# Performance work log

Hardware: AMD Instinct MI355X
Metric: run time of the kernel (lower is better)

The kernel has to match this reference:

```python
import math
import jax, jax.numpy as jnp
import numpy as np

C = 64
GRID = 2

def _conv1x1(x, W, b):
    # 1x1 conv == channel-mixing matmul: [B,C,H,W] x [O,C] -> [B,O,H,W]
    return jnp.einsum('bchw,oc->bohw', x, W) + b[None, :, None, None]

def setup_inputs() -> dict:
    key = jax.random.key(0)
    ks = jax.random.split(key, 11)
    s = 1.0 / math.sqrt(C)
    def w(k):
        return jax.random.normal(k, (C, C), dtype=jnp.float32) * s
    def bias(k):
        return jax.random.normal(k, (C,), dtype=jnp.float32) * 0.02
    return {
        'x': jax.random.normal(ks[0], (2, C, 128, 128), dtype=jnp.float32),
        'Wq': w(ks[1]), 'bq': bias(ks[2]),
        'Wk': w(ks[3]), 'bk': bias(ks[4]),
        'Wa': w(ks[5]), 'ba': bias(ks[6]),
        'Wb': w(ks[7]), 'bb': bias(ks[8]),
        'Wo': w(ks[9]), 'bo': bias(ks[10]),
    }

def reference(x, Wq, bq, Wk, bk, Wa, ba, Wb, bb, Wo, bo):
    B, c, H, W = x.shape
    g = GRID
    rh, rw = H // g, W // g  # H,W chosen divisible by grid -> no reflect pad
    N = rh * rw
    R = g * g

    q = _conv1x1(x, Wq, bq)
    k = _conv1x1(x, Wk, bk)
    a = _conv1x1(x, Wa, ba)
    bt = _conv1x1(x, Wb, bb)

    def regionize(t):
        # [B,C,H,W] -> [B, R, C, N] with N = rh*rw row-major per region
        return t.reshape(B, c, g, rh, g, rw).transpose(0, 2, 4, 1, 3, 5).reshape(B, R, c, N)

    qr, kr, ar, br = regionize(q), regionize(k), regionize(a), regionize(bt)

    # attn[b,r,n,m] = softmax_m( q^T k / sqrt(C) )
    attn = jax.nn.softmax(jnp.einsum('brcn,brcm->brnm', qr, kr) / math.sqrt(c), axis=-1)

    # out_r = alpha @ attn + beta @ attn^T
    out = (jnp.einsum('brcj,brjm->brcm', ar, attn)
           + jnp.einsum('brcj,brmj->brcm', br, attn))

    # [B,R,C,N] -> [B,C,H,W]
    out = out.reshape(B, g, g, c, rh, rw).transpose(0, 3, 1, 4, 2, 5).reshape(B, c, H, W)
    return _conv1x1(out, Wo, bo)
```

## Files before the change

kernel.cpp:

```cpp
#include <hip/hip_runtime.h>


typedef __attribute__((ext_vector_type(8)))  short bf16x8;
typedef __attribute__((ext_vector_type(16))) float f32x16;

#define MFMA32(a, b, c) __builtin_amdgcn_mfma_f32_32x32x16_bf16(a, b, c, 0, 0, 0)

constexpr int REG_ELEMS = 4096 * 64;
constexpr size_t QP_OFF  = 0;
constexpr size_t KP_OFF  = 4u  << 20;
constexpr size_t ATL_OFF = 8u  << 20;
constexpr size_t BTL_OFF = 12u << 20;
constexpr size_t OUTP_OFF= 16u << 20;
constexpr size_t LNV_OFF = 20u << 20;

constexpr float QSCALE = 0.18033688011112042f;

__device__ __forceinline__ short f2bf(float f) {
    union { float f; unsigned u; } v; v.f = f;
    unsigned r = v.u + 0x7fffu + ((v.u >> 16) & 1u);
    return (short)(r >> 16);
}
__device__ __forceinline__ float bf2f(short s) {
    union { unsigned u; float f; } v; v.u = ((unsigned)(unsigned short)s) << 16;
    return v.f;
}
__device__ __forceinline__ unsigned fbits(float f) {
    union { float f; unsigned u; } v; v.f = f; return v.u;
}
__device__ __forceinline__ unsigned pack_trunc(float e0, float e1) {
    return __builtin_amdgcn_perm(fbits(e1), fbits(e0), 0x07060302u);
}
__device__ __forceinline__ f32x16 zero16() {
    f32x16 z;
    #pragma unroll
    for (int i = 0; i < 16; ++i) z[i] = 0.f;
    return z;
}
__device__ __forceinline__ float fexp2(float x) {
#if __has_builtin(__builtin_amdgcn_exp2f)
    return __builtin_amdgcn_exp2f(x);
#else
    return exp2f(x);
#endif
}
__device__ __forceinline__ void permswap32(unsigned& a, unsigned& b, bool hi) {
#if __has_builtin(__builtin_amdgcn_permlane32_swap)
    auto r = __builtin_amdgcn_permlane32_swap(a, b, false, false);
    a = r[0]; b = r[1];
#elif __has_builtin(__builtin_amdgcn_permlane32_swap_b32)
    auto r = __builtin_amdgcn_permlane32_swap_b32(a, b, false, false);
    a = r[0]; b = r[1];
#else
    unsigned ax = (unsigned)__shfl_xor((int)a, 32);
    unsigned bx = (unsigned)__shfl_xor((int)b, 32);
    unsigned na = hi ? bx : a;
    unsigned nb = hi ? b  : ax;
    a = na; b = nb;
#endif
}

typedef __attribute__((address_space(1))) const unsigned char as1_t;
typedef __attribute__((address_space(3))) unsigned char as3_t;
__device__ __forceinline__ void stage16(const void* g, void* l) {
    __builtin_amdgcn_global_load_lds((as1_t*)g, (as3_t*)l, 16, 0, 0);
}

__global__ __launch_bounds__(256) void k_conv_in(
    const float* __restrict__ x,
    const float* __restrict__ Wq, const float* __restrict__ bq,
    const float* __restrict__ Wk, const float* __restrict__ bk,
    const float* __restrict__ Wa, const float* __restrict__ ba,
    const float* __restrict__ Wb, const float* __restrict__ bb,
    char* __restrict__ ws)
{
    const int tid  = threadIdx.x;
    const int blk  = blockIdx.x;
    const int wseg = blk & 1;
    const int h    = (blk >> 1) & 127;
    const int b    = blk >> 8;
    const int br   = b * 4 + (h >> 6) * 2 + wseg;
    const int n0   = (h & 63) * 64;

    __shared__ float xs[64][68];
    __shared__ short trans[2][64][72];

    const float* xp = x + ((size_t)b * 64 * 16384) + (size_t)h * 128 + wseg * 64;
    #pragma unroll
    for (int r = 0; r < 4; ++r) {
        int idx = r * 256 + tid;
        int c   = idx >> 4;
        int w4  = (idx & 15) << 2;
        *(float4*)&xs[c][w4] = *(const float4*)(xp + (size_t)c * 16384 + w4);
    }
    __syncthreads();

    const int lane = tid & 63;
    const int wid  = tid >> 6;
    const int col  = lane & 31;
    const int l5   = lane >> 5;
    const int pH   = wid & 1;
    const int oH   = wid >> 1;
    const int px   = pH * 32 + col;
    const int oc   = oH * 32 + col;

    bf16x8 xhi[4], xlo[4];
    #pragma unroll
    for (int s = 0; s < 4; ++s) {
        union { bf16x8 v; short sh[8]; } uh, ul;
        #pragma unroll
        for (int e = 0; e < 8; ++e) {
            float xv = xs[s * 16 + l5 * 8 + e][px];
            short hh = f2bf(xv);
            uh.sh[e] = hh;
            ul.sh[e] = f2bf(xv - bf2f(hh));
        }
        xhi[s] = uh.v; xlo[s] = ul.v;
    }

    #pragma unroll
    for (int mat = 0; mat < 4; ++mat) {
        const float* Wsel = (mat == 0) ? Wq : (mat == 1) ? Wk : (mat == 2) ? Wa : Wb;
        const float* bsel = (mat == 0) ? bq : (mat == 1) ? bk : (mat == 2) ? ba : bb;

        bf16x8 whi[4], wlo[4];
        const float* wrow = Wsel + (size_t)oc * 64;
        #pragma unroll
        for (int s = 0; s < 4; ++s) {
            float4 f0 = *(const float4*)(wrow + s * 16 + l5 * 8);
            float4 f1 = *(const float4*)(wrow + s * 16 + l5 * 8 + 4);
            float wf[8] = { f0.x, f0.y, f0.z, f0.w, f1.x, f1.y, f1.z, f1.w };
            union { bf16x8 v; short sh[8]; } uh, ul;
            #pragma unroll
            for (int e = 0; e < 8; ++e) {
                short hh = f2bf(wf[e]);
                uh.sh[e] = hh;
                ul.sh[e] = f2bf(wf[e] - bf2f(hh));
            }
            whi[s] = uh.v; wlo[s] = ul.v;
        }

        f32x16 d = zero16();
        #pragma unroll
        for (int s = 0; s < 4; ++s) {
            d = MFMA32(xhi[s], whi[s], d);
            d = MFMA32(xhi[s], wlo[s], d);
            d = MFMA32(xlo[s], whi[s], d);
        }

        const float bias = bsel[oc];
        if (mat < 2) {
            const float sc = (mat == 0) ? QSCALE : 1.0f;
            #pragma unroll
            for (int r = 0; r < 16; ++r) {
                int pxl = pH * 32 + (r & 3) + 8 * (r >> 2) + 4 * l5;
                trans[mat][pxl][oc] = f2bf((d[r] + bias) * sc);
            }
        } else {
            short* base = (short*)(ws + (mat == 2 ? ATL_OFF : BTL_OFF))
                          + (size_t)br * REG_ELEMS;
            const int sw   = (oc >> 1) & 3;
            const int tile = (n0 >> 5) + pH;
            #pragma unroll
            for (int q = 0; q < 4; ++q) {
                short tmp4[4];
                #pragma unroll
                for (int rr = 0; rr < 4; ++rr) tmp4[rr] = f2bf(d[4 * q + rr] + bias);
                int segp = q ^ sw;
                short* p = base + (size_t)tile * 2048 + oc * 32 + segp * 8 + 4 * l5;
                *(uint2*)p = *(uint2*)tmp4;
            }
        }
    }
    __syncthreads();

    #pragma unroll
    for (int rep = 0; rep < 4; ++rep) {
        int idx  = rep * 256 + tid;
        int mat2 = idx >> 9;
        int row  = (idx >> 3) & 63;
        int seg  = idx & 7;
        short* dst = (short*)(ws + (mat2 ? KP_OFF : QP_OFF))
                     + (size_t)br * REG_ELEMS + (size_t)(n0 + row) * 64
                     + (seg ^ (row & 7)) * 8;
        *(uint4*)dst = *(uint4*)&trans[mat2][row][seg * 8];
    }
}

__global__ __launch_bounds__(256, 2) void k_stats(char* __restrict__ ws)
{
    const int tid  = threadIdx.x;
    const int br   = blockIdx.x & 7;
    const int nt   = blockIdx.x >> 3;
    const int lane = tid & 63;
    const int w    = tid >> 6;
    const int wn   = w & 1;
    const int wi   = w >> 1;
    const int col  = lane & 31;
    const int l5   = lane >> 5;

    const short* Qb  = (const short*)(ws + QP_OFF) + (size_t)br * REG_ELEMS;
    const char*  Kbb = ws + KP_OFF + (size_t)br * REG_ELEMS * 2;

    __shared__ __align__(16) char smem[17408];

    const int nrow = nt * 64 + wn * 32 + col;
    bf16x8 afr[4];
    #pragma unroll
    for (int s = 0; s < 4; ++s)
        afr[s] = *(const bf16x8*)(Qb + (size_t)nrow * 64 + (((2*s+l5) ^ (col & 7)) * 8));

    float sm[16];
    #pragma unroll
    for (int r = 0; r < 16; ++r) sm[r] = 0.f;

    {
        const char* g = Kbb + (size_t)w * 2048 + lane * 16;
        char* l = smem + w * 2048;
        stage16(g, l); stage16(g + 1024, l + 1024);
    }

    #pragma unroll 2
    for (int slab = 0; slab < 64; ++slab) {
        __syncthreads();
        if (slab + 1 < 64) {
            const char* g = Kbb + (size_t)(slab + 1) * 8192 + w * 2048 + lane * 16;
            char* l = smem + ((slab + 1) & 1) * 8192 + w * 2048;
            stage16(g, l); stage16(g + 1024, l + 1024);
        }
        const short* Ks = (const short*)(smem + (slab & 1) * 8192);
        f32x16 d = zero16();
        #pragma unroll
        for (int s = 0; s < 4; ++s) {
            bf16x8 bf = *(const bf16x8*)(Ks + (wi * 32 + col) * 64
                                         + ((2*s+l5) ^ (col & 7)) * 8);
            d = MFMA32(afr[s], bf, d);
        }
        #pragma unroll
        for (int r = 0; r < 16; ++r) sm[r] += fexp2(d[r]);
    }

    #pragma unroll
    for (int off = 1; off < 32; off <<= 1)
        #pragma unroll
        for (int r = 0; r < 16; ++r) sm[r] += __shfl_xor(sm[r], off);

    __syncthreads();
    float* Lred = (float*)(smem + 16384);
    float* Larr = (float*)(smem + 16896);
    if (col == 0) {
        #pragma unroll
        for (int r = 0; r < 16; ++r)
            Lred[w * 32 + ((r & 3) + 8 * (r >> 2) + 4 * l5)] = sm[r];
    }
    __syncthreads();
    if (tid < 64) {
        int wn2 = tid >> 5, nl = tid & 31;
        float L = Lred[wn2 * 32 + nl] + Lred[(wn2 + 2) * 32 + nl];
        float li = 1.0f / L;
        Larr[tid] = li;
        ((float*)(ws + LNV_OFF))[(size_t)br * 4096 + nt * 64 + tid] = li;
    }
    __syncthreads();

    short* Ab = (short*)(ws + ATL_OFF) + (size_t)br * REG_ELEMS + (size_t)nt * 4096;
    #pragma unroll
    for (int rep = 0; rep < 2; ++rep) {
        int id = rep * 256 + tid;
        int t = id >> 8, c = (id >> 2) & 63, s = id & 3;
        int sg = s ^ ((c >> 1) & 3);
        int jl = t * 32 + sg * 8;
        short* p = Ab + (size_t)t * 2048 + c * 32 + s * 8;
        uint4 v = *(uint4*)p;
        short* sp = (short*)&v;
        short o[8];
        #pragma unroll
        for (int e = 0; e < 8; ++e) o[e] = f2bf(bf2f(sp[e]) * Larr[jl + e]);
        *(uint4*)p = *(uint4*)o;
    }
}

__global__ __launch_bounds__(256, 2) void k_attn(char* __restrict__ ws)
{
    const int tid  = threadIdx.x;
    const int br   = blockIdx.x & 7;
    const int mt   = blockIdx.x >> 3;
    const int lane = tid & 63;
    const int w    = tid >> 6;
    const int wm   = w & 1;
    const int wj   = w >> 1;
    const int col  = lane & 31;
    const int l5   = lane >> 5;
    const bool hi  = (l5 != 0);

    const char* Qbb = ws + QP_OFF  + (size_t)br * REG_ELEMS * 2;
    const char* Kbb = ws + KP_OFF  + (size_t)br * REG_ELEMS * 2;
    const char* Abb = ws + ATL_OFF + (size_t)br * REG_ELEMS * 2;
    const char* Bbb = ws + BTL_OFF + (size_t)br * REG_ELEMS * 2;
    const float* Lnv = (const float*)(ws + LNV_OFF) + (size_t)br * 4096;
    short* OutPb    = (short*)(ws + OUTP_OFF) + (size_t)br * REG_ELEMS;

    __shared__ __align__(16) char smem[32768];

    const int mrow = mt * 64 + wm * 32 + col;
    const short* msrc = (const short*)(wj == 0 ? Kbb : Qbb) + (size_t)mrow * 64;
    bf16x8 mf[4];
    #pragma unroll
    for (int s = 0; s < 4; ++s)
        mf[s] = *(const bf16x8*)(msrc + ((2*s+l5) ^ (col & 7)) * 8);

    f32x16 accL = zero16(), accH = zero16();

    const char* gsb = (w == 0) ? Qbb : (w == 1) ? Kbb : (w == 2) ? Abb : Bbb;

    {
        const char* g = gsb + lane * 16;
        char* l = smem + w * 4096 + lane * 16;
        #pragma unroll
        for (int i = 0; i < 4; ++i) stage16(g + i * 1024, l + i * 1024);
    }

    #pragma unroll 2
    for (int slab = 0; slab < 128; ++slab) {
        __syncthreads();
        if (slab + 1 < 128) {
            const char* g = gsb + (size_t)(slab + 1) * 4096 + lane * 16;
            char* l = smem + ((slab + 1) & 1) * 16384 + w * 4096 + lane * 16;
            #pragma unroll
            for (int i = 0; i < 4; ++i) stage16(g + i * 1024, l + i * 1024);
        }
        const char* sb = smem + (slab & 1) * 16384;
        const short* js = (const short*)(sb + (wj == 0 ? 0 : 4096));
        const short* ts = (const short*)(sb + (wj == 0 ? 8192 : 12288));

        f32x16 d = zero16();
        #pragma unroll
        for (int s = 0; s < 4; ++s) {
            bf16x8 a = *(const bf16x8*)(js + col * 64 + ((2*s+l5) ^ (col & 7)) * 8);
            d = MFMA32(a, mf[s], d);
        }

        unsigned Wp[8];
        #pragma unroll
        for (int q = 0; q < 4; ++q) {
            Wp[2*q]   = pack_trunc(fexp2(d[4*q]),   fexp2(d[4*q+1]));
            Wp[2*q+1] = pack_trunc(fexp2(d[4*q+2]), fexp2(d[4*q+3]));
        }

        #pragma unroll
        for (int k16 = 0; k16 < 2; ++k16) {
            unsigned u0 = Wp[4*k16+0], u1 = Wp[4*k16+1];
            unsigned u2 = Wp[4*k16+2], u3 = Wp[4*k16+3];
            permswap32(u0, u2, hi);
            permswap32(u1, u3, hi);
            union { uint4 u; bf16x8 v; } fr;
            fr.u.x = u0; fr.u.y = u1; fr.u.z = u2; fr.u.w = u3;

            const int swz = ((2*k16 + l5) ^ ((col >> 1) & 3)) * 8;
            bf16x8 bL = *(const bf16x8*)(ts + col * 32 + swz);
            bf16x8 bH = *(const bf16x8*)(ts + (col + 32) * 32 + swz);
            accL = MFMA32(fr.v, bL, accL);
            accH = MFMA32(fr.v, bH, accH);
        }
    }

    __syncthreads();
    float* red = (float*)smem;
    if (wj == 0) {
        #pragma unroll
        for (int r = 0; r < 16; ++r) {
            int ml = wm * 32 + (r & 3) + 8 * (r >> 2) + 4 * l5;
            red[ml * 68 + col]      = accL[r];
            red[ml * 68 + 32 + col] = accH[r];
        }
    }
    __syncthreads();
    if (wj == 1) {
        #pragma unroll
        for (int r = 0; r < 16; ++r) {
            int ml = wm * 32 + (r & 3) + 8 * (r >> 2) + 4 * l5;
            float li = Lnv[mt * 64 + ml];
            red[ml * 68 + col]      += li * accL[r];
            red[ml * 68 + 32 + col] += li * accH[r];
        }
    }
    __syncthreads();
    {
        const int m  = tid >> 2;
        const int c0 = (tid & 3) * 16;
        const float* rp = red + m * 68 + c0;
        uint4 p0, p1;
        p0.x = pack_trunc(rp[0],  rp[1]);  p0.y = pack_trunc(rp[2],  rp[3]);
        p0.z = pack_trunc(rp[4],  rp[5]);  p0.w = pack_trunc(rp[6],  rp[7]);
        p1.x = pack_trunc(rp[8],  rp[9]);  p1.y = pack_trunc(rp[10], rp[11]);
        p1.z = pack_trunc(rp[12], rp[13]); p1.w = pack_trunc(rp[14], rp[15]);
        short* orow = OutPb + (size_t)(mt * 64 + m) * 64 + c0;
        *(uint4*)orow       = p0;
        *(uint4*)(orow + 8) = p1;
    }
}

__global__ __launch_bounds__(64) void k_conv_out(
    const char* __restrict__ ws,
    const float* __restrict__ Wo, const float* __restrict__ bo,
    float* __restrict__ out)
{
    const int lane = threadIdx.x;
    const int br   = blockIdx.x & 7;
    const int nt   = blockIdx.x >> 3;
    const int col  = lane & 31;
    const int l5   = lane >> 5;

    const short* OutPb = (const short*)(ws + OUTP_OFF) + (size_t)br * REG_ELEMS;

    bf16x8 afr[4];
    const short* arow = OutPb + (size_t)(nt * 32 + col) * 64 + l5 * 8;
    #pragma unroll
    for (int s = 0; s < 4; ++s) afr[s] = *(const bf16x8*)(arow + s * 16);

    bf16x8 bw[2][4];
    #pragma unroll
    for (int oh = 0; oh < 2; ++oh) {
        const float* wrow = Wo + (size_t)(oh * 32 + col) * 64 + l5 * 8;
        #pragma unroll
        for (int s = 0; s < 4; ++s) {
            float4 f0 = *(const float4*)(wrow + s * 16);
            float4 f1 = *(const float4*)(wrow + s * 16 + 4);
            union { bf16x8 v; short sh[8]; } u;
            u.sh[0] = f2bf(f0.x); u.sh[1] = f2bf(f0.y);
            u.sh[2] = f2bf(f0.z); u.sh[3] = f2bf(f0.w);
            u.sh[4] = f2bf(f1.x); u.sh[5] = f2bf(f1.y);
            u.sh[6] = f2bf(f1.z); u.sh[7] = f2bf(f1.w);
            bw[oh][s] = u.v;
        }
    }

    f32x16 d0 = zero16(), d1 = zero16();
    #pragma unroll
    for (int s = 0; s < 4; ++s) {
        d0 = MFMA32(afr[s], bw[0][s], d0);
        d1 = MFMA32(afr[s], bw[1][s], d1);
    }

    const int b  = br >> 2;
    const int gi = (br >> 1) & 1;
    const int gj = br & 1;

    #pragma unroll
    for (int oh = 0; oh < 2; ++oh) {
        const int oc = oh * 32 + col;
        const float bias = bo[oc];
        const f32x16& d = oh ? d1 : d0;
        #pragma unroll
        for (int q = 0; q < 4; ++q) {
            int nloc = 8 * q + 4 * l5;
            int nreg = nt * 32 + nloc;
            int wp   = nreg & 63;
            int ip   = nreg >> 6;
            float4 v = make_float4(d[4*q+0] + bias, d[4*q+1] + bias,
                                   d[4*q+2] + bias, d[4*q+3] + bias);
            float* op = out + ((size_t)(b * 64 + oc)) * 16384
                        + (size_t)(gi * 64 + ip) * 128 + gj * 64 + wp;
            *(float4*)op = v;
        }
    }
}

extern "C" void kernel_launch(void* const* d_in, const int* in_sizes, int n_in,
                              void* d_out, int out_size, void* d_ws, size_t ws_size,
                              hipStream_t stream)
{
    const float* x  = (const float*)d_in[0];
    const float* Wq = (const float*)d_in[1];
    const float* bq = (const float*)d_in[2];
    const float* Wk = (const float*)d_in[3];
    const float* bk = (const float*)d_in[4];
    const float* Wa = (const float*)d_in[5];
    const float* ba = (const float*)d_in[6];
    const float* Wb = (const float*)d_in[7];
    const float* bb = (const float*)d_in[8];
    const float* Wo = (const float*)d_in[9];
    const float* bo = (const float*)d_in[10];
    char* ws   = (char*)d_ws;
    float* out = (float*)d_out;

    hipLaunchKernelGGL(k_conv_in,  dim3(512),  dim3(256), 0, stream,
                       x, Wq, bq, Wk, bk, Wa, ba, Wb, bb, ws);
    hipLaunchKernelGGL(k_stats,    dim3(512),  dim3(256), 0, stream, ws);
    hipLaunchKernelGGL(k_attn,     dim3(512),  dim3(256), 0, stream, ws);
    hipLaunchKernelGGL(k_conv_out, dim3(1024), dim3(64),  0, stream,
                       ws, Wo, bo, out);
}
```

Before: 206.1 us.

## Split key dimension across two blocks in stats and attention kernels

Doubles the grid of k_stats and k_attn by splitting the 4096-long key/j range into two halves. Partial softmax denominators are written separately and merged by a new small k_stats2 kernel. The in-place rescaling of the alpha tile by 1/L is dropped; that normalization is instead applied inside k_attn to the exp weights on the alpha path. Two partial attention outputs are summed in k_conv_out via extra MFMAs. This raises occupancy on a 256-CU device (512 blocks was only 2 per CU), at the cost of an extra launch, double output buffers and per-slab Lnv loads.

```diff
diff --git a/kernel.cpp b/kernel.cpp
--- a/kernel.cpp
+++ b/kernel.cpp
@@ -7,12 +7,14 @@
 #define MFMA32(a, b, c) __builtin_amdgcn_mfma_f32_32x32x16_bf16(a, b, c, 0, 0, 0)
 
 constexpr int REG_ELEMS = 4096 * 64;
-constexpr size_t QP_OFF  = 0;
-constexpr size_t KP_OFF  = 4u  << 20;
-constexpr size_t ATL_OFF = 8u  << 20;
-constexpr size_t BTL_OFF = 12u << 20;
-constexpr size_t OUTP_OFF= 16u << 20;
-constexpr size_t LNV_OFF = 20u << 20;
+constexpr size_t QP_OFF    = 0;
+constexpr size_t KP_OFF    = 4u  << 20;
+constexpr size_t ATL_OFF   = 8u  << 20;
+constexpr size_t BTL_OFF   = 12u << 20;
+constexpr size_t OUTP0_OFF = 16u << 20;
+constexpr size_t OUTP1_OFF = 20u << 20;
+constexpr size_t LNV_OFF   = 24u << 20;
+constexpr size_t LPART_OFF = (24u << 20) + (128u << 10);
 
 constexpr float QSCALE = 0.18033688011112042f;
 
@@ -191,7 +193,8 @@
 {
     const int tid  = threadIdx.x;
     const int br   = blockIdx.x & 7;
-    const int nt   = blockIdx.x >> 3;
+    const int nt   = (blockIdx.x >> 3) & 63;
+    const int ms   = blockIdx.x >> 9;
     const int lane = tid & 63;
     const int w    = tid >> 6;
     const int wn   = w & 1;
@@ -200,9 +203,10 @@
     const int l5   = lane >> 5;
 
     const short* Qb  = (const short*)(ws + QP_OFF) + (size_t)br * REG_ELEMS;
-    const char*  Kbb = ws + KP_OFF + (size_t)br * REG_ELEMS * 2;
-
-    __shared__ __align__(16) char smem[17408];
+    const char*  Kbb = ws + KP_OFF + (size_t)br * REG_ELEMS * 2
+                       + (size_t)ms * 262144;
+
+    __shared__ __align__(16) char smem[16896];
 
     const int nrow = nt * 64 + wn * 32 + col;
     bf16x8 afr[4];
@@ -221,9 +225,9 @@
     }
 
     #pragma unroll 2
-    for (int slab = 0; slab < 64; ++slab) {
+    for (int slab = 0; slab < 32; ++slab) {
         __syncthreads();
-        if (slab + 1 < 64) {
+        if (slab + 1 < 32) {
             const char* g = Kbb + (size_t)(slab + 1) * 8192 + w * 2048 + lane * 16;
             char* l = smem + ((slab + 1) & 1) * 8192 + w * 2048;
             stage16(g, l); stage16(g + 1024, l + 1024);
@@ -247,7 +251,6 @@
 
     __syncthreads();
     float* Lred = (float*)(smem + 16384);
-    float* Larr = (float*)(smem + 16896);
     if (col == 0) {
         #pragma unroll
         for (int r = 0; r < 16; ++r)
@@ -257,34 +260,24 @@
     if (tid < 64) {
         int wn2 = tid >> 5, nl = tid & 31;
         float L = Lred[wn2 * 32 + nl] + Lred[(wn2 + 2) * 32 + nl];
-        float li = 1.0f / L;
-        Larr[tid] = li;
-        ((float*)(ws + LNV_OFF))[(size_t)br * 4096 + nt * 64 + tid] = li;
-    }
-    __syncthreads();
-
-    short* Ab = (short*)(ws + ATL_OFF) + (size_t)br * REG_ELEMS + (size_t)nt * 4096;
-    #pragma unroll
-    for (int rep = 0; rep < 2; ++rep) {
-        int id = rep * 256 + tid;
-        int t = id >> 8, c = (id >> 2) & 63, s = id & 3;
-        int sg = s ^ ((c >> 1) & 3);
-        int jl = t * 32 + sg * 8;
-        short* p = Ab + (size_t)t * 2048 + c * 32 + s * 8;
-        uint4 v = *(uint4*)p;
-        short* sp = (short*)&v;
-        short o[8];
-        #pragma unroll
-        for (int e = 0; e < 8; ++e) o[e] = f2bf(bf2f(sp[e]) * Larr[jl + e]);
-        *(uint4*)p = *(uint4*)o;
-    }
+        ((float*)(ws + LPART_OFF))[(size_t)ms * 32768 + (size_t)br * 4096
+                                   + nt * 64 + tid] = L;
+    }
+}
+
+__global__ __launch_bounds__(256) void k_stats2(char* __restrict__ ws)
+{
+    const int i = blockIdx.x * 256 + threadIdx.x;
+    const float* Lp = (const float*)(ws + LPART_OFF);
+    ((float*)(ws + LNV_OFF))[i] = 1.0f / (Lp[i] + Lp[32768 + i]);
 }
 
 __global__ __launch_bounds__(256, 2) void k_attn(char* __restrict__ ws)
 {
     const int tid  = threadIdx.x;
     const int br   = blockIdx.x & 7;
-    const int mt   = blockIdx.x >> 3;
+    const int mt   = (blockIdx.x >> 3) & 63;
+    const int js   = blockIdx.x >> 9;
     const int lane = tid & 63;
     const int w    = tid >> 6;
     const int wm   = w & 1;
@@ -298,7 +291,7 @@
     const char* Abb = ws + ATL_OFF + (size_t)br * REG_ELEMS * 2;
     const char* Bbb = ws + BTL_OFF + (size_t)br * REG_ELEMS * 2;
     const float* Lnv = (const float*)(ws + LNV_OFF) + (size_t)br * 4096;
-    short* OutPb    = (short*)(ws + OUTP_OFF) + (size_t)br * REG_ELEMS;
+    short* OutPb = (short*)(ws + (js ? OUTP1_OFF : OUTP0_OFF)) + (size_t)br * REG_ELEMS;
 
     __shared__ __align__(16) char smem[32768];
 
@@ -311,7 +304,8 @@
 
     f32x16 accL = zero16(), accH = zero16();
 
-    const char* gsb = (w == 0) ? Qbb : (w == 1) ? Kbb : (w == 2) ? Abb : Bbb;
+    const char* gsb = ((w == 0) ? Qbb : (w == 1) ? Kbb : (w == 2) ? Abb : Bbb)
+                      + (size_t)js * 262144;
 
     {
         const char* g = gsb + lane * 16;
@@ -321,30 +315,40 @@
     }
 
     #pragma unroll 2
-    for (int slab = 0; slab < 128; ++slab) {
+    for (int slab = 0; slab < 64; ++slab) {
         __syncthreads();
-        if (slab + 1 < 128) {
+        if (slab + 1 < 64) {
             const char* g = gsb + (size_t)(slab + 1) * 4096 + lane * 16;
             char* l = smem + ((slab + 1) & 1) * 16384 + w * 4096 + lane * 16;
             #pragma unroll
             for (int i = 0; i < 4; ++i) stage16(g + i * 1024, l + i * 1024);
         }
         const char* sb = smem + (slab & 1) * 16384;
-        const short* js = (const short*)(sb + (wj == 0 ? 0 : 4096));
-        const short* ts = (const short*)(sb + (wj == 0 ? 8192 : 12288));
+        const short* js_ = (const short*)(sb + (wj == 0 ? 0 : 4096));
+        const short* ts  = (const short*)(sb + (wj == 0 ? 8192 : 12288));
 
         f32x16 d = zero16();
         #pragma unroll
         for (int s = 0; s < 4; ++s) {
-            bf16x8 a = *(const bf16x8*)(js + col * 64 + ((2*s+l5) ^ (col & 7)) * 8);
+            bf16x8 a = *(const bf16x8*)(js_ + col * 64 + ((2*s+l5) ^ (col & 7)) * 8);
             d = MFMA32(a, mf[s], d);
         }
 
         unsigned Wp[8];
-        #pragma unroll
-        for (int q = 0; q < 4; ++q) {
-            Wp[2*q]   = pack_trunc(fexp2(d[4*q]),   fexp2(d[4*q+1]));
-            Wp[2*q+1] = pack_trunc(fexp2(d[4*q+2]), fexp2(d[4*q+3]));
+        if (wj == 0) {
+            const int jbase = (js * 64 + slab) * 32;
+            #pragma unroll
+            for (int q = 0; q < 4; ++q) {
+                float4 Lq = *(const float4*)(Lnv + jbase + 8 * q + 4 * l5);
+                Wp[2*q]   = pack_trunc(fexp2(d[4*q])   * Lq.x, fexp2(d[4*q+1]) * Lq.y);
+                Wp[2*q+1] = pack_trunc(fexp2(d[4*q+2]) * Lq.z, fexp2(d[4*q+3]) * Lq.w);
+            }
+        } else {
+            #pragma unroll
+            for (int q = 0; q < 4; ++q) {
+                Wp[2*q]   = pack_trunc(fexp2(d[4*q]),   fexp2(d[4*q+1]));
+                Wp[2*q+1] = pack_trunc(fexp2(d[4*q+2]), fexp2(d[4*q+3]));
+            }
         }
 
         #pragma unroll
@@ -411,12 +415,16 @@
     const int col  = lane & 31;
     const int l5   = lane >> 5;
 
-    const short* OutPb = (const short*)(ws + OUTP_OFF) + (size_t)br * REG_ELEMS;
-
-    bf16x8 afr[4];
-    const short* arow = OutPb + (size_t)(nt * 32 + col) * 64 + l5 * 8;
-    #pragma unroll
-    for (int s = 0; s < 4; ++s) afr[s] = *(const bf16x8*)(arow + s * 16);
+    const short* O0 = (const short*)(ws + OUTP0_OFF) + (size_t)br * REG_ELEMS;
+    const short* O1 = (const short*)(ws + OUTP1_OFF) + (size_t)br * REG_ELEMS;
+
+    bf16x8 af0[4], af1[4];
+    const size_t aoff = (size_t)(nt * 32 + col) * 64 + l5 * 8;
+    #pragma unroll
+    for (int s = 0; s < 4; ++s) {
+        af0[s] = *(const bf16x8*)(O0 + aoff + s * 16);
+        af1[s] = *(const bf16x8*)(O1 + aoff + s * 16);
+    }
 
     bf16x8 bw[2][4];
     #pragma unroll
@@ -438,8 +446,10 @@
     f32x16 d0 = zero16(), d1 = zero16();
     #pragma unroll
     for (int s = 0; s < 4; ++s) {
-        d0 = MFMA32(afr[s], bw[0][s], d0);
-        d1 = MFMA32(afr[s], bw[1][s], d1);
+        d0 = MFMA32(af0[s], bw[0][s], d0);
+        d0 = MFMA32(af1[s], bw[0][s], d0);
+        d1 = MFMA32(af0[s], bw[1][s], d1);
+        d1 = MFMA32(af1[s], bw[1][s], d1);
     }
 
     const int b  = br >> 2;
@@ -486,8 +496,9 @@
 
     hipLaunchKernelGGL(k_conv_in,  dim3(512),  dim3(256), 0, stream,
                        x, Wq, bq, Wk, bk, Wa, ba, Wb, bb, ws);
-    hipLaunchKernelGGL(k_stats,    dim3(512),  dim3(256), 0, stream, ws);
-    hipLaunchKernelGGL(k_attn,     dim3(512),  dim3(256), 0, stream, ws);
+    hipLaunchKernelGGL(k_stats,    dim3(1024), dim3(256), 0, stream, ws);
+    hipLaunchKernelGGL(k_stats2,   dim3(128),  dim3(256), 0, stream, ws);
+    hipLaunchKernelGGL(k_attn,     dim3(1024), dim3(256), 0, stream, ws);
     hipLaunchKernelGGL(k_conv_out, dim3(1024), dim3(64),  0, stream,
                        ws, Wo, bo, out);
 }
```

Measured after the change: 212.0 us. 2.8% more time.

## Fold inverse-sum scaling of alpha into attn kernel; pack conv_out into 256-thread blocks

Applied to the files above, without the earlier changes.

The k_stats kernel no longer rescales the alpha tile in global memory by 1/L. Only the inverse row sums are stored, and k_attn multiplies the exp weights by them for the wj==0 warps (alpha path) before packing to bf16. This removes a read-modify-write pass over the alpha buffer and an extra barrier, at the cost of extra global loads and multiplies inside the attention loop. Separately, k_conv_out now packs four 64-thread tiles into each 256-thread block to cut the block count.

```diff
diff --git a/kernel.cpp b/kernel.cpp
--- a/kernel.cpp
+++ b/kernel.cpp
@@ -202,7 +202,7 @@
     const short* Qb  = (const short*)(ws + QP_OFF) + (size_t)br * REG_ELEMS;
     const char*  Kbb = ws + KP_OFF + (size_t)br * REG_ELEMS * 2;
 
-    __shared__ __align__(16) char smem[17408];
+    __shared__ __align__(16) char smem[16896];
 
     const int nrow = nt * 64 + wn * 32 + col;
     bf16x8 afr[4];
@@ -247,7 +247,6 @@
 
     __syncthreads();
     float* Lred = (float*)(smem + 16384);
-    float* Larr = (float*)(smem + 16896);
     if (col == 0) {
         #pragma unroll
         for (int r = 0; r < 16; ++r)
@@ -257,26 +256,7 @@
     if (tid < 64) {
         int wn2 = tid >> 5, nl = tid & 31;
         float L = Lred[wn2 * 32 + nl] + Lred[(wn2 + 2) * 32 + nl];
-        float li = 1.0f / L;
-        Larr[tid] = li;
-        ((float*)(ws + LNV_OFF))[(size_t)br * 4096 + nt * 64 + tid] = li;
-    }
-    __syncthreads();
-
-    short* Ab = (short*)(ws + ATL_OFF) + (size_t)br * REG_ELEMS + (size_t)nt * 4096;
-    #pragma unroll
-    for (int rep = 0; rep < 2; ++rep) {
-        int id = rep * 256 + tid;
-        int t = id >> 8, c = (id >> 2) & 63, s = id & 3;
-        int sg = s ^ ((c >> 1) & 3);
-        int jl = t * 32 + sg * 8;
-        short* p = Ab + (size_t)t * 2048 + c * 32 + s * 8;
-        uint4 v = *(uint4*)p;
-        short* sp = (short*)&v;
-        short o[8];
-        #pragma unroll
-        for (int e = 0; e < 8; ++e) o[e] = f2bf(bf2f(sp[e]) * Larr[jl + e]);
-        *(uint4*)p = *(uint4*)o;
+        ((float*)(ws + LNV_OFF))[(size_t)br * 4096 + nt * 64 + tid] = 1.0f / L;
     }
 }
 
@@ -341,10 +321,20 @@
         }
 
         unsigned Wp[8];
-        #pragma unroll
-        for (int q = 0; q < 4; ++q) {
-            Wp[2*q]   = pack_trunc(fexp2(d[4*q]),   fexp2(d[4*q+1]));
-            Wp[2*q+1] = pack_trunc(fexp2(d[4*q+2]), fexp2(d[4*q+3]));
+        if (wj == 0) {
+            const int jbase = slab * 32;
+            #pragma unroll
+            for (int q = 0; q < 4; ++q) {
+                float4 Lq = *(const float4*)(Lnv + jbase + 8 * q + 4 * l5);
+                Wp[2*q]   = pack_trunc(fexp2(d[4*q])   * Lq.x, fexp2(d[4*q+1]) * Lq.y);
+                Wp[2*q+1] = pack_trunc(fexp2(d[4*q+2]) * Lq.z, fexp2(d[4*q+3]) * Lq.w);
+            }
+        } else {
+            #pragma unroll
+            for (int q = 0; q < 4; ++q) {
+                Wp[2*q]   = pack_trunc(fexp2(d[4*q]),   fexp2(d[4*q+1]));
+                Wp[2*q+1] = pack_trunc(fexp2(d[4*q+2]), fexp2(d[4*q+3]));
+            }
         }
 
         #pragma unroll
@@ -400,14 +390,17 @@
     }
 }
 
-__global__ __launch_bounds__(64) void k_conv_out(
+__global__ __launch_bounds__(256) void k_conv_out(
     const char* __restrict__ ws,
     const float* __restrict__ Wo, const float* __restrict__ bo,
     float* __restrict__ out)
 {
-    const int lane = threadIdx.x;
-    const int br   = blockIdx.x & 7;
-    const int nt   = blockIdx.x >> 3;
+    const int tid  = threadIdx.x;
+    const int lane = tid & 63;
+    const int sub  = tid >> 6;
+    const int blk  = blockIdx.x;
+    const int br   = blk & 7;
+    const int nt   = (blk >> 3) * 4 + sub;
     const int col  = lane & 31;
     const int l5   = lane >> 5;
 
@@ -484,10 +477,10 @@
     char* ws   = (char*)d_ws;
     float* out = (float*)d_out;
 
-    hipLaunchKernelGGL(k_conv_in,  dim3(512),  dim3(256), 0, stream,
+    hipLaunchKernelGGL(k_conv_in,  dim3(512), dim3(256), 0, stream,
                        x, Wq, bq, Wk, bk, Wa, ba, Wb, bb, ws);
-    hipLaunchKernelGGL(k_stats,    dim3(512),  dim3(256), 0, stream, ws);
-    hipLaunchKernelGGL(k_attn,     dim3(512),  dim3(256), 0, stream, ws);
-    hipLaunchKernelGGL(k_conv_out, dim3(1024), dim3(64),  0, stream,
+    hipLaunchKernelGGL(k_stats,    dim3(512), dim3(256), 0, stream, ws);
+    hipLaunchKernelGGL(k_attn,     dim3(512), dim3(256), 0, stream, ws);
+    hipLaunchKernelGGL(k_conv_out, dim3(256), dim3(256), 0, stream,
                        ws, Wo, bo, out);
 }
```

Measured after the change: 238.0 us. 15.5% more time.

## Split attention reduction over j into two halves, combine partials in output conv

Applied to the files above, without the earlier changes.

The attention kernel's 128-slab reduction is split into two halves across twice as many blocks, each writing partial outputs to separate workspace buffers. The output conv kernel now loads both partials and accumulates them via extra MFMAs, and is relaunched with 256-thread blocks covering four tiles each. This raises parallelism from 512 to 1024 attention blocks to better fill the GPU, at the cost of extra partial-output traffic and bf16 rounding of each partial before summation.

```diff
diff --git a/kernel.cpp b/kernel.cpp
--- a/kernel.cpp
+++ b/kernel.cpp
@@ -7,12 +7,13 @@
 #define MFMA32(a, b, c) __builtin_amdgcn_mfma_f32_32x32x16_bf16(a, b, c, 0, 0, 0)
 
 constexpr int REG_ELEMS = 4096 * 64;
-constexpr size_t QP_OFF  = 0;
-constexpr size_t KP_OFF  = 4u  << 20;
-constexpr size_t ATL_OFF = 8u  << 20;
-constexpr size_t BTL_OFF = 12u << 20;
-constexpr size_t OUTP_OFF= 16u << 20;
-constexpr size_t LNV_OFF = 20u << 20;
+constexpr size_t QP_OFF    = 0;
+constexpr size_t KP_OFF    = 4u  << 20;
+constexpr size_t ATL_OFF   = 8u  << 20;
+constexpr size_t BTL_OFF   = 12u << 20;
+constexpr size_t OUTP0_OFF = 16u << 20;
+constexpr size_t OUTP1_OFF = 20u << 20;
+constexpr size_t LNV_OFF   = 24u << 20;
 
 constexpr float QSCALE = 0.18033688011112042f;
 
@@ -284,7 +285,8 @@
 {
     const int tid  = threadIdx.x;
     const int br   = blockIdx.x & 7;
-    const int mt   = blockIdx.x >> 3;
+    const int mt   = (blockIdx.x >> 3) & 63;
+    const int js   = blockIdx.x >> 9;
     const int lane = tid & 63;
     const int w    = tid >> 6;
     const int wm   = w & 1;
@@ -298,7 +300,7 @@
     const char* Abb = ws + ATL_OFF + (size_t)br * REG_ELEMS * 2;
     const char* Bbb = ws + BTL_OFF + (size_t)br * REG_ELEMS * 2;
     const float* Lnv = (const float*)(ws + LNV_OFF) + (size_t)br * 4096;
-    short* OutPb    = (short*)(ws + OUTP_OFF) + (size_t)br * REG_ELEMS;
+    short* OutPb = (short*)(ws + (js ? OUTP1_OFF : OUTP0_OFF)) + (size_t)br * REG_ELEMS;
 
     __shared__ __align__(16) char smem[32768];
 
@@ -311,7 +313,8 @@
 
     f32x16 accL = zero16(), accH = zero16();
 
-    const char* gsb = (w == 0) ? Qbb : (w == 1) ? Kbb : (w == 2) ? Abb : Bbb;
+    const char* gsb = ((w == 0) ? Qbb : (w == 1) ? Kbb : (w == 2) ? Abb : Bbb)
+                      + (size_t)js * 262144;
 
     {
         const char* g = gsb + lane * 16;
@@ -321,22 +324,22 @@
     }
 
     #pragma unroll 2
-    for (int slab = 0; slab < 128; ++slab) {
+    for (int slab = 0; slab < 64; ++slab) {
         __syncthreads();
-        if (slab + 1 < 128) {
+        if (slab + 1 < 64) {
             const char* g = gsb + (size_t)(slab + 1) * 4096 + lane * 16;
             char* l = smem + ((slab + 1) & 1) * 16384 + w * 4096 + lane * 16;
             #pragma unroll
             for (int i = 0; i < 4; ++i) stage16(g + i * 1024, l + i * 1024);
         }
         const char* sb = smem + (slab & 1) * 16384;
-        const short* js = (const short*)(sb + (wj == 0 ? 0 : 4096));
+        const short* jr = (const short*)(sb + (wj == 0 ? 0 : 4096));
         const short* ts = (const short*)(sb + (wj == 0 ? 8192 : 12288));
 
         f32x16 d = zero16();
         #pragma unroll
         for (int s = 0; s < 4; ++s) {
-            bf16x8 a = *(const bf16x8*)(js + col * 64 + ((2*s+l5) ^ (col & 7)) * 8);
+            bf16x8 a = *(const bf16x8*)(jr + col * 64 + ((2*s+l5) ^ (col & 7)) * 8);
             d = MFMA32(a, mf[s], d);
         }
 
@@ -400,23 +403,30 @@
     }
 }
 
-__global__ __launch_bounds__(64) void k_conv_out(
+__global__ __launch_bounds__(256) void k_conv_out(
     const char* __restrict__ ws,
     const float* __restrict__ Wo, const float* __restrict__ bo,
     float* __restrict__ out)
 {
-    const int lane = threadIdx.x;
-    const int br   = blockIdx.x & 7;
-    const int nt   = blockIdx.x >> 3;
+    const int tid  = threadIdx.x;
+    const int lane = tid & 63;
+    const int sub  = tid >> 6;
+    const int blk  = blockIdx.x;
+    const int br   = blk & 7;
+    const int nt   = (blk >> 3) * 4 + sub;
     const int col  = lane & 31;
     const int l5   = lane >> 5;
 
-    const short* OutPb = (const short*)(ws + OUTP_OFF) + (size_t)br * REG_ELEMS;
-
-    bf16x8 afr[4];
-    const short* arow = OutPb + (size_t)(nt * 32 + col) * 64 + l5 * 8;
-    #pragma unroll
-    for (int s = 0; s < 4; ++s) afr[s] = *(const bf16x8*)(arow + s * 16);
+    const short* O0 = (const short*)(ws + OUTP0_OFF) + (size_t)br * REG_ELEMS;
+    const short* O1 = (const short*)(ws + OUTP1_OFF) + (size_t)br * REG_ELEMS;
+
+    bf16x8 af0[4], af1[4];
+    const size_t aoff = (size_t)(nt * 32 + col) * 64 + l5 * 8;
+    #pragma unroll
+    for (int s = 0; s < 4; ++s) {
+        af0[s] = *(const bf16x8*)(O0 + aoff + s * 16);
+        af1[s] = *(const bf16x8*)(O1 + aoff + s * 16);
+    }
 
     bf16x8 bw[2][4];
     #pragma unroll
@@ -438,8 +448,10 @@
     f32x16 d0 = zero16(), d1 = zero16();
     #pragma unroll
     for (int s = 0; s < 4; ++s) {
-        d0 = MFMA32(afr[s], bw[0][s], d0);
-        d1 = MFMA32(afr[s], bw[1][s], d1);
+        d0 = MFMA32(af0[s], bw[0][s], d0);
+        d0 = MFMA32(af1[s], bw[0][s], d0);
+        d1 = MFMA32(af0[s], bw[1][s], d1);
+        d1 = MFMA32(af1[s], bw[1][s], d1);
     }
 
     const int b  = br >> 2;
@@ -487,7 +499,7 @@
     hipLaunchKernelGGL(k_conv_in,  dim3(512),  dim3(256), 0, stream,
                        x, Wq, bq, Wk, bk, Wa, ba, Wb, bb, ws);
     hipLaunchKernelGGL(k_stats,    dim3(512),  dim3(256), 0, stream, ws);
-    hipLaunchKernelGGL(k_attn,     dim3(512),  dim3(256), 0, stream, ws);
-    hipLaunchKernelGGL(k_conv_out, dim3(1024), dim3(64),  0, stream,
+    hipLaunchKernelGGL(k_attn,     dim3(1024), dim3(256), 0, stream, ws);
+    hipLaunchKernelGGL(k_conv_out, dim3(256),  dim3(256), 0, stream,
                        ws, Wo, bo, out);
 }
```

Result: no change. 208.5 us (+1.2%).
